# Kernel optimization log

Hardware: AMD Instinct MI355X
Metric: run time of the kernel (lower is better)

The kernel has to match this reference:

```python
import jax, jax.numpy as jnp
import numpy as np

N, E, H = 5000, 40000, 8
DIMS = [(258, 512), (516, 256), (262, 128), (136, 20)]  # (in_feature, out_feature) per GATDeformer


def setup_inputs() -> dict:
    key = jax.random.key(0)
    ks = jax.random.split(key, 10)
    s = 0.05
    data = jax.random.normal(ks[0], (N, 10), jnp.float32)
    src = jax.random.randint(ks[1], (E,), 0, N)
    off = jax.random.randint(ks[2], (E,), 1, N)
    edge_idx = jnp.stack([src, (src + off) % N]).astype(jnp.int32)  # no self loops by construction
    inp = {
        'data': data,
        'edge_idx': edge_idx,
        'W0': jax.random.normal(ks[3], (10, 256), jnp.float32) * s,
        'b0': jnp.zeros((256,), jnp.float32),
    }
    for i, (din, dout) in enumerate(DIMS, start=1):
        k = jax.random.split(ks[3 + i], 3)
        inp[f'W{i}'] = jax.random.normal(k[0], (din, H * dout), jnp.float32) * s
        inp[f'asrc{i}'] = jax.random.normal(k[1], (H, dout), jnp.float32) * s
        inp[f'adst{i}'] = jax.random.normal(k[2], (H, dout), jnp.float32) * s
        inp[f'bias{i}'] = jnp.zeros((dout,), jnp.float32)
    return inp


def _gat(x, src, dst, W, a_s, a_d, b):
    """PyG GATConv (concat=False): returns (mean-over-heads output + bias, alpha [E',H])."""
    Hh, C = a_s.shape
    h = (x @ W).reshape(N, Hh, C)                               # [N,H,C]
    e_s = jnp.einsum('nhc,hc->nh', h, a_s)                      # [N,H]
    e_d = jnp.einsum('nhc,hc->nh', h, a_d)
    logits = jax.nn.leaky_relu(e_s[src] + e_d[dst], 0.2)        # [E',H]
    m = jax.ops.segment_max(logits, dst, num_segments=N)        # segment softmax over incoming edges
    ex = jnp.exp(logits - m[dst])
    alpha = ex / jax.ops.segment_sum(ex, dst, num_segments=N)[dst]
    out = jax.ops.segment_sum(alpha[:, :, None] * h[src], dst, num_segments=N)  # [N,H,C]
    return out.mean(axis=1) + b, alpha


def _deformer(af, src, dst, W, a_s, a_d, b):
    # find_boundary on the layer input features
    up, down = af[:, 0] == 1.0, af[:, 0] == 0.0
    left, right = af[:, 1] == 0.0, af[:, 1] == 1.0
    feat, alpha = _gat(af, src, dst, W, a_s, a_d, b)
    coord = af[:, :2]
    # second propagate: alpha*0.2 reused to aggregate source coordinates, then mean over heads
    msg = (alpha * 0.2)[:, :, None] * coord[src][:, None, :]    # [E',H,2]
    oc = jax.ops.segment_sum(msg, dst, num_segments=N).mean(axis=1)
    # fix_boundary (sequential overwrite order: up then down, left then right)
    c0 = jnp.where(down, 0.0, jnp.where(up, 1.0, oc[:, 0]))
    c1 = jnp.where(right, 1.0, jnp.where(left, 0.0, oc[:, 1]))
    return jnp.stack([c0, c1], axis=1), jax.nn.selu(feat)


def reference(data, edge_idx, W0, b0, W1, asrc1, adst1, bias1, W2, asrc2, adst2, bias2, W3, asrc3, adst3, bias3, W4, asrc4, adst4, bias4):
    sl = jnp.arange(N, dtype=edge_idx.dtype)
    src = jnp.concatenate([edge_idx[0], sl])   # GATConv add_self_loops=True
    dst = jnp.concatenate([edge_idx[1], sl])
    coord = data[:, :2]
    feat = jax.nn.selu(data @ W0 + b0)
    c1_, f1 = _deformer(jnp.concatenate([coord, feat], 1), src, dst, W1, asrc1, adst1, bias1)
    c2_, f2 = _deformer(jnp.concatenate([c1_, coord, f1], 1), src, dst, W2, asrc2, adst2, bias2)
    c3_, f3 = _deformer(jnp.concatenate([c2_, c1_, coord, f2], 1), src, dst, W3, asrc3, adst3, bias3)
    c4_, _ = _deformer(jnp.concatenate([c3_, c2_, c1_, coord, f3], 1), src, dst, W4, asrc4, adst4, bias4)
    return c4_
```

## Files before the change

kernel.cpp:

```cpp
#include <hip/hip_runtime.h>

#define N_NODES 5000
#define NH 8

typedef unsigned short u16;
typedef short bf16x8 __attribute__((ext_vector_type(8)));
typedef float f32x4 __attribute__((ext_vector_type(4)));

static __device__ __forceinline__ float selu_f(float x) {
    const float sc = 1.0507009873554805f;
    const float al = 1.6732632423543772f;
    return x > 0.f ? sc * x : sc * al * (__expf(x) - 1.f);
}

static __device__ __forceinline__ u16 f2bf(float x) {
    union { float f; unsigned u; } v; v.f = x;
    unsigned r = v.u + 0x7fff + ((v.u >> 16) & 1);
    return (u16)(r >> 16);
}

static __device__ __forceinline__ float bf2f(unsigned hi16) {
    union { unsigned u; float f; } v; v.u = hi16 << 16;
    return v.f;
}

#define GL2LDS16(gp, lp)                                                        \
    __builtin_amdgcn_global_load_lds(                                           \
        (const __attribute__((address_space(1))) void*)(gp),                    \
        (__attribute__((address_space(3))) void*)(lp), 16, 0, 0)

__global__ void k_count(const int* __restrict__ ei, int* cnt, int E, int Esz) {
    int e = blockIdx.x * 256 + threadIdx.x;
    if (e >= Esz) return;
    int dst = (e < E) ? ei[E + e] : (e - E);
    atomicAdd(&cnt[dst], 1);
}

__global__ void k_scan(const int* __restrict__ cnt, int* __restrict__ rowp, int n) {
    __shared__ int ps[256];
    int t = threadIdx.x;
    int per = (n + 255) / 256;
    int b = t * per;
    int s = 0;
    for (int i = 0; i < per; ++i) { int idx = b + i; if (idx < n) s += cnt[idx]; }
    ps[t] = s;
    __syncthreads();
    for (int off = 1; off < 256; off <<= 1) {
        int v = (t >= off) ? ps[t - off] : 0;
        __syncthreads();
        ps[t] += v;
        __syncthreads();
    }
    int run = (t == 0) ? 0 : ps[t - 1];
    for (int i = 0; i < per; ++i) {
        int idx = b + i;
        if (idx < n) { rowp[idx] = run; run += cnt[idx]; }
    }
    if (t == 255) rowp[n] = run;
}

__global__ void k_fill(const int* __restrict__ ei, const int* __restrict__ rowp,
                       int* cur, int* ssrc, int E, int Esz) {
    int e = blockIdx.x * 256 + threadIdx.x;
    if (e >= Esz) return;
    int src, dst;
    if (e < E) { src = ei[e]; dst = ei[E + e]; }
    else       { src = e - E; dst = src; }
    int pos = rowp[dst] + atomicAdd(&cur[dst], 1);
    ssrc[pos] = src;
}

__global__ __launch_bounds__(256) void k_prep(
        const float* W1, const float* W2, const float* W3, const float* W4,
        const float* s1, const float* s2, const float* s3, const float* s4,
        const float* d1, const float* d2, const float* d3, const float* d4,
        float* __restrict__ fsAll, float* __restrict__ fdAll,
        u16* T1, u16* T2, u16* T3) {
    const int Ks[4] = {258, 516, 262, 136};
    const int Cs[4] = {512, 256, 128, 20};
    int bid = blockIdx.x;
    if (bid < 516) {
        int li = bid / 129;
        int k = (bid % 129) * 4 + (threadIdx.x >> 6);
        int lane = threadIdx.x & 63;
        if (k >= Ks[li]) return;
        const float* W  = (li == 0) ? W1 : (li == 1) ? W2 : (li == 2) ? W3 : W4;
        const float* as = (li == 0) ? s1 : (li == 1) ? s2 : (li == 2) ? s3 : s4;
        const float* ad = (li == 0) ? d1 : (li == 1) ? d2 : (li == 2) ? d3 : d4;
        int C = Cs[li];
        float s[8] = {0.f,0.f,0.f,0.f,0.f,0.f,0.f,0.f};
        float d[8] = {0.f,0.f,0.f,0.f,0.f,0.f,0.f,0.f};
        const float* wr = W + (size_t)k * 8 * C;
        for (int c = lane; c < C; c += 64) {
            #pragma unroll
            for (int h = 0; h < 8; ++h) {
                float w = wr[h * C + c];
                s[h] += w * as[h * C + c];
                d[h] += w * ad[h * C + c];
            }
        }
        #pragma unroll
        for (int off = 32; off >= 1; off >>= 1) {
            #pragma unroll
            for (int h = 0; h < 8; ++h) {
                s[h] += __shfl_xor(s[h], off);
                d[h] += __shfl_xor(d[h], off);
            }
        }
        if (lane == 0) {
            float* fo = fsAll + (size_t)li * 516 * 8 + k * 8;
            float* go = fdAll + (size_t)li * 516 * 8 + k * 8;
            #pragma unroll
            for (int h = 0; h < 8; ++h) { fo[h] = s[h]; go[h] = d[h]; }
        }
    } else {
        const int Kps[3] = {288, 544, 288};
        int w = bid - 516;
        int li = w / (16 * 136);
        int rem = w % (16 * 136);
        int c0 = (rem % 16) * 32;
        int j0 = (rem / 16) * 32;
        int C = Cs[li], K = Ks[li], Kp = Kps[li], KK = 8 * Kp;
        if (c0 >= C || j0 >= KK) return;
        const float* W = (li == 0) ? W1 : (li == 1) ? W2 : W3;
        u16* Wt2 = (li == 0) ? T1 : (li == 1) ? T2 : T3;
        __shared__ float tile[32][33];
        int h = j0 / Kp, k0 = j0 % Kp;
        int tid = threadIdx.x;
        for (int idx = tid; idx < 1024; idx += 256) {
            int kr = idx >> 5, cc = idx & 31;
            int gk = k0 + kr;
            tile[kr][cc] = (gk < K) ? W[(size_t)gk * (8 * C) + h * C + c0 + cc] : 0.f;
        }
        __syncthreads();
        for (int idx = tid; idx < 1024; idx += 256) {
            int cr = idx >> 5, kc = idx & 31;
            Wt2[(size_t)(c0 + cr) * KK + j0 + kc] = f2bf(tile[kc][cr]);
        }
    }
}

__global__ __launch_bounds__(256) void k_mf(const float* p0, const float* p1,
                                            const float* p2, const float* p3, int np,
                                            const float* __restrict__ data,
                                            const float* __restrict__ W0,
                                            const float* __restrict__ b0,
                                            const u16* __restrict__ facc,
                                            const float* __restrict__ biasp,
                                            int split, int MN, int FC, int K, int Kp,
                                            const float* __restrict__ fs,
                                            const float* __restrict__ fd,
                                            u16* __restrict__ afb,
                                            float* __restrict__ es, float* __restrict__ ed,
                                            float* __restrict__ c0out) {
    int n = blockIdx.x, t = threadIdx.x;
    __shared__ float drow[10];
    bool l1 = (biasp == nullptr);
    if (l1 && t < 10) drow[t] = data[n * 10 + t];
    __syncthreads();
    float pes[8] = {0.f,0.f,0.f,0.f,0.f,0.f,0.f,0.f};
    float ped[8] = {0.f,0.f,0.f,0.f,0.f,0.f,0.f,0.f};
    u16* rowb = afb + (size_t)n * Kp;
    for (int cf2 = t; 2 * cf2 < FC; cf2 += 256) {
        int cf = 2 * cf2;
        float v0, v1;
        if (l1) {
            float2 bb = *(const float2*)(b0 + cf);
            v0 = bb.x; v1 = bb.y;
            #pragma unroll
            for (int k = 0; k < 10; ++k) {
                float2 ww = *(const float2*)(W0 + k * 256 + cf);
                v0 += drow[k] * ww.x;
                v1 += drow[k] * ww.y;
            }
            v0 = selu_f(v0); v1 = selu_f(v1);
        } else {
            float s0 = 0.f, s1 = 0.f;
            for (int z = 0; z < split; ++z) {
                unsigned pr = *(const unsigned*)(facc + (size_t)z * MN + (size_t)n * FC + cf);
                s0 += bf2f(pr & 0xffff);
                s1 += bf2f(pr >> 16);
            }
            float2 bb = *(const float2*)(biasp + cf);
            v0 = selu_f(s0 * 0.125f + bb.x);
            v1 = selu_f(s1 * 0.125f + bb.y);
        }
        int c = 2 * np + cf;
        *(unsigned*)(rowb + c) = (unsigned)f2bf(v0) | ((unsigned)f2bf(v1) << 16);
        const float* fsr = fs + c * 8;
        const float* fdr = fd + c * 8;
        #pragma unroll
        for (int h = 0; h < 8; ++h) {
            pes[h] += v0 * fsr[h] + v1 * fsr[8 + h];
            ped[h] += v0 * fdr[h] + v1 * fdr[8 + h];
        }
    }
    if (t < 2 * np) {
        float v;
        if (l1) {
            v = drow[t];
            c0out[n * 2 + t] = v;
        } else {
            const float* p = (t < 2) ? p0 : (t < 4) ? p1 : (t < 6) ? p2 : p3;
            v = p[n * 2 + (t & 1)];
        }
        rowb[t] = f2bf(v);
        #pragma unroll
        for (int h = 0; h < 8; ++h) { pes[h] += v * fs[t * 8 + h]; ped[h] += v * fd[t * 8 + h]; }
    }
    for (int c = K + t; c < Kp; c += 256) rowb[c] = 0;
    #pragma unroll
    for (int off = 32; off >= 1; off >>= 1) {
        #pragma unroll
        for (int h = 0; h < 8; ++h) {
            pes[h] += __shfl_xor(pes[h], off);
            ped[h] += __shfl_xor(ped[h], off);
        }
    }
    __shared__ float red[4][16];
    int wv = t >> 6, ln = t & 63;
    if (ln == 0) {
        #pragma unroll
        for (int h = 0; h < 8; ++h) { red[wv][h] = pes[h]; red[wv][8 + h] = ped[h]; }
    }
    __syncthreads();
    if (t < 16) {
        float s = red[0][t] + red[1][t] + red[2][t] + red[3][t];
        if (t < 8) es[n * 8 + t] = s;
        else       ed[n * 8 + (t - 8)] = s;
    }
}

template <int S32>
__global__ __launch_bounds__(256) void k_gag(const float* __restrict__ es,
                            const float* __restrict__ ed,
                            const int* __restrict__ rowp, const int* __restrict__ ssrc,
                            const float* __restrict__ cprev, const u16* __restrict__ afb,
                            u16* __restrict__ g, float* __restrict__ cnext, int Kp) {
    __shared__ int   ls[128];
    __shared__ float la[128 * 8];
    __shared__ float lc0[128], lc1[128], lw[128];
    __shared__ float linv[8];
    int n = blockIdx.x, t = threadIdx.x;
    int s0 = rowp[n];
    int deg = rowp[n + 1] - s0;
    if (deg > 128) deg = 128;
    for (int i = t; i < deg; i += 256) {
        int src = ssrc[s0 + i];
        ls[i] = src;
        lc0[i] = cprev[src * 2];
        lc1[i] = cprev[src * 2 + 1];
    }
    __syncthreads();
    for (int i = t; i < deg * 8; i += 256) {
        int e = i >> 3, h = i & 7;
        float x = es[ls[e] * 8 + h] + ed[n * 8 + h];
        la[i] = x > 0.f ? x : 0.2f * x;
    }
    __syncthreads();
    if (t < 8) {
        float m = -1e30f;
        for (int e = 0; e < deg; ++e) m = fmaxf(m, la[e * 8 + t]);
        float s = 0.f;
        for (int e = 0; e < deg; ++e) {
            float v = __expf(la[e * 8 + t] - m);
            la[e * 8 + t] = v;
            s += v;
        }
        linv[t] = 1.f / s;
    }
    __syncthreads();
    for (int i = t; i < deg; i += 256) {
        float w = 0.f;
        #pragma unroll
        for (int h = 0; h < 8; ++h) w += la[i * 8 + h] * linv[h];
        lw[i] = w;
    }
    int nW = Kp >> 1;
    float acc[8][2 * S32];
    #pragma unroll
    for (int h = 0; h < 8; ++h)
        #pragma unroll
        for (int s = 0; s < 2 * S32; ++s) acc[h][s] = 0.f;
    int e = 0;
    for (; e + 3 < deg; e += 4) {
        const unsigned* r0 = (const unsigned*)(afb + (size_t)ls[e] * Kp);
        const unsigned* r1 = (const unsigned*)(afb + (size_t)ls[e + 1] * Kp);
        const unsigned* r2 = (const unsigned*)(afb + (size_t)ls[e + 2] * Kp);
        const unsigned* r3 = (const unsigned*)(afb + (size_t)ls[e + 3] * Kp);
        unsigned v0[S32], v1[S32], v2[S32], v3[S32];
        #pragma unroll
        for (int s = 0; s < S32; ++s) {
            int w = t + 256 * s;
            bool ok = (w < nW);
            v0[s] = ok ? r0[w] : 0u;
            v1[s] = ok ? r1[w] : 0u;
            v2[s] = ok ? r2[w] : 0u;
            v3[s] = ok ? r3[w] : 0u;
        }
        float a0[8], a1[8], a2[8], a3[8];
        #pragma unroll
        for (int h = 0; h < 8; ++h) {
            a0[h] = la[(e + 0) * 8 + h];
            a1[h] = la[(e + 1) * 8 + h];
            a2[h] = la[(e + 2) * 8 + h];
            a3[h] = la[(e + 3) * 8 + h];
        }
        #pragma unroll
        for (int s = 0; s < S32; ++s) {
            float x0 = bf2f(v0[s] & 0xffff), y0 = bf2f(v0[s] >> 16);
            float x1 = bf2f(v1[s] & 0xffff), y1 = bf2f(v1[s] >> 16);
            float x2 = bf2f(v2[s] & 0xffff), y2 = bf2f(v2[s] >> 16);
            float x3 = bf2f(v3[s] & 0xffff), y3 = bf2f(v3[s] >> 16);
            #pragma unroll
            for (int h = 0; h < 8; ++h) {
                acc[h][2 * s]     += a0[h] * x0 + a1[h] * x1 + a2[h] * x2 + a3[h] * x3;
                acc[h][2 * s + 1] += a0[h] * y0 + a1[h] * y1 + a2[h] * y2 + a3[h] * y3;
            }
        }
    }
    for (; e < deg; ++e) {
        const unsigned* r0 = (const unsigned*)(afb + (size_t)ls[e] * Kp);
        unsigned v0[S32];
        #pragma unroll
        for (int s = 0; s < S32; ++s) {
            int w = t + 256 * s;
            v0[s] = (w < nW) ? r0[w] : 0u;
        }
        float a0[8];
        #pragma unroll
        for (int h = 0; h < 8; ++h) a0[h] = la[e * 8 + h];
        #pragma unroll
        for (int s = 0; s < S32; ++s) {
            float x0 = bf2f(v0[s] & 0xffff), y0 = bf2f(v0[s] >> 16);
            #pragma unroll
            for (int h = 0; h < 8; ++h) {
                acc[h][2 * s]     += a0[h] * x0;
                acc[h][2 * s + 1] += a0[h] * y0;
            }
        }
    }
    unsigned* grw = (unsigned*)(g + (size_t)n * 8 * Kp);
    #pragma unroll
    for (int s = 0; s < S32; ++s) {
        int w = t + 256 * s;
        if (w < nW) {
            #pragma unroll
            for (int h = 0; h < 8; ++h) {
                float iv = linv[h];
                unsigned lo = f2bf(acc[h][2 * s] * iv);
                unsigned hi = f2bf(acc[h][2 * s + 1] * iv);
                grw[h * nW + w] = lo | (hi << 16);
            }
        }
    }
    __syncthreads();
    if (t == 0) {
        float oc0 = 0.f, oc1 = 0.f;
        for (int i = 0; i < deg; ++i) { oc0 += lw[i] * lc0[i]; oc1 += lw[i] * lc1[i]; }
        oc0 *= 0.025f; oc1 *= 0.025f;
        float a0 = cprev[n * 2], a1 = cprev[n * 2 + 1];
        cnext[n * 2]     = (a0 == 0.f) ? 0.f : ((a0 == 1.f) ? 1.f : oc0);
        cnext[n * 2 + 1] = (a1 == 1.f) ? 1.f : ((a1 == 0.f) ? 0.f : oc1);
    }
}

__global__ __launch_bounds__(256) void k_gemm_s(const u16* __restrict__ A,
                                                const u16* __restrict__ Bt,
                                                u16* __restrict__ facc16,
                                                int M, int KK, int NC, int kchunk, int MN) {
    __shared__ u16 As[3][128 * 32];
    __shared__ u16 Bs[3][128 * 32];
    int tid = threadIdx.x;
    int wave = tid >> 6, lane = tid & 63;
    int bm = blockIdx.y * 128, bn = blockIdx.x * 128, z = blockIdx.z;
    int kbeg = z * kchunk, kend = min(KK, kbeg + kchunk);
    int wm = (wave >> 1) * 64, wn = (wave & 1) * 64;
    int l16 = lane & 15, q = lane >> 4;
    f32x4 acc[4][4] = {};

    int seg0 = wave * 128 + lane;
    int seg1 = seg0 + 64;
    int row0 = seg0 >> 2, sq0 = (seg0 & 3) ^ (row0 & 3);
    int row1 = seg1 >> 2, sq1 = (seg1 & 3) ^ (row1 & 3);
    const u16* ga0 = A  + (size_t)(bm + row0) * KK + sq0 * 8;
    const u16* ga1 = A  + (size_t)(bm + row1) * KK + sq1 * 8;
    const u16* gb0 = Bt + (size_t)(bn + row0) * KK + sq0 * 8;
    const u16* gb1 = Bt + (size_t)(bn + row1) * KK + sq1 * 8;
    int lo0 = (wave * 2 + 0) * 512;
    int lo1 = (wave * 2 + 1) * 512;

#define STAGE_T(buf, kk)                          \
    do {                                          \
        GL2LDS16(ga0 + (kk), &As[buf][lo0]);      \
        GL2LDS16(ga1 + (kk), &As[buf][lo1]);      \
        GL2LDS16(gb0 + (kk), &Bs[buf][lo0]);      \
        GL2LDS16(gb1 + (kk), &Bs[buf][lo1]);      \
    } while (0)

    STAGE_T(0, kbeg);
    if (kbeg + 32 < kend) STAGE_T(1, kbeg + 32);
    int cur = 0;
    for (int k0 = kbeg; k0 < kend; k0 += 32) {
        if (k0 + 64 < kend) {
            int nb = cur + 2; if (nb >= 3) nb -= 3;
            STAGE_T(nb, k0 + 64);
            asm volatile("s_waitcnt vmcnt(8)" ::: "memory");
        } else if (k0 + 32 < kend) {
            asm volatile("s_waitcnt vmcnt(4)" ::: "memory");
        } else {
            asm volatile("s_waitcnt vmcnt(0)" ::: "memory");
        }
        __builtin_amdgcn_s_barrier();
        const u16* Asr = As[cur];
        const u16* Bsr = Bs[cur];
        bf16x8 fa[4], fb[4];
        #pragma unroll
        for (int mi = 0; mi < 4; ++mi) {
            int row = wm + mi * 16 + l16;
            fa[mi] = *(const bf16x8*)(Asr + row * 32 + ((q ^ (row & 3)) * 8));
            int col = wn + mi * 16 + l16;
            fb[mi] = *(const bf16x8*)(Bsr + col * 32 + ((q ^ (col & 3)) * 8));
        }
        #pragma unroll
        for (int mi = 0; mi < 4; ++mi)
            #pragma unroll
            for (int ni = 0; ni < 4; ++ni)
                acc[mi][ni] = __builtin_amdgcn_mfma_f32_16x16x32_bf16(fa[mi], fb[ni], acc[mi][ni], 0, 0, 0);
        __builtin_amdgcn_s_barrier();
        cur += 1; if (cur >= 3) cur -= 3;
    }
#undef STAGE_T
    u16* out = facc16 + (size_t)z * MN;
    #pragma unroll
    for (int mi = 0; mi < 4; ++mi) {
        int row0s = bm + wm + mi * 16 + q * 4;
        #pragma unroll
        for (int ni = 0; ni < 4; ++ni) {
            int col = bn + wn + ni * 16 + l16;
            #pragma unroll
            for (int r = 0; r < 4; ++r) {
                int row = row0s + r;
                if (row < M) out[(size_t)row * NC + col] = f2bf(acc[mi][ni][r]);
            }
        }
    }
}

__global__ void k_final(const float* __restrict__ es, const float* __restrict__ ed,
                        const int* __restrict__ rowp, const int* __restrict__ ssrc,
                        const float* __restrict__ cprev, float* __restrict__ outp) {
    int wid = (blockIdx.x * blockDim.x + threadIdx.x) >> 6;
    int lane = threadIdx.x & 63;
    if (wid >= N_NODES) return;
    int n = wid;
    int s0 = rowp[n], deg = rowp[n + 1] - s0;
    int h = lane & 7, ei = lane >> 3;
    float edh = ed[n * 8 + h];
    float m = -1e30f;
    for (int b = 0; b < deg; b += 8) {
        int e = b + ei;
        if (e < deg) {
            int src = ssrc[s0 + e];
            float x = es[src * 8 + h] + edh;
            x = x > 0.f ? x : 0.2f * x;
            m = fmaxf(m, x);
        }
    }
    m = fmaxf(m, __shfl_xor(m, 8));
    m = fmaxf(m, __shfl_xor(m, 16));
    m = fmaxf(m, __shfl_xor(m, 32));
    float ssum = 0.f;
    for (int b = 0; b < deg; b += 8) {
        int e = b + ei;
        if (e < deg) {
            int src = ssrc[s0 + e];
            float x = es[src * 8 + h] + edh;
            x = x > 0.f ? x : 0.2f * x;
            ssum += __expf(x - m);
        }
    }
    ssum += __shfl_xor(ssum, 8);
    ssum += __shfl_xor(ssum, 16);
    ssum += __shfl_xor(ssum, 32);
    float inv = 1.f / ssum;
    float oc0 = 0.f, oc1 = 0.f;
    for (int b = 0; b < deg; b += 8) {
        int e = b + ei;
        if (e < deg) {
            int src = ssrc[s0 + e];
            float x = es[src * 8 + h] + edh;
            x = x > 0.f ? x : 0.2f * x;
            float w = __expf(x - m) * inv;
            w += __shfl_xor(w, 1);
            w += __shfl_xor(w, 2);
            w += __shfl_xor(w, 4);
            if (h == 0) {
                oc0 += w * cprev[src * 2];
                oc1 += w * cprev[src * 2 + 1];
            }
        }
    }
    oc0 += __shfl_xor(oc0, 8);  oc1 += __shfl_xor(oc1, 8);
    oc0 += __shfl_xor(oc0, 16); oc1 += __shfl_xor(oc1, 16);
    oc0 += __shfl_xor(oc0, 32); oc1 += __shfl_xor(oc1, 32);
    if (lane == 0) {
        oc0 *= 0.025f; oc1 *= 0.025f;
        float a0 = cprev[n * 2], a1 = cprev[n * 2 + 1];
        outp[n * 2]     = (a0 == 0.f) ? 0.f : ((a0 == 1.f) ? 1.f : oc0);
        outp[n * 2 + 1] = (a1 == 1.f) ? 1.f : ((a1 == 0.f) ? 0.f : oc1);
    }
}

extern "C" void kernel_launch(void* const* d_in, const int* in_sizes, int n_in,
                              void* d_out, int out_size, void* d_ws, size_t ws_size,
                              hipStream_t stream) {
    const float* data = (const float*)d_in[0];
    const int* ei = (const int*)d_in[1];
    const float* W0 = (const float*)d_in[2];
    const float* b0 = (const float*)d_in[3];
    int E = in_sizes[1] / 2;
    int Esz = E + N_NODES;

    char* wp = (char*)d_ws;
    size_t off = 0;
    auto alloc = [&](size_t bytes) {
        void* p = wp + off;
        off += (bytes + 1023) & ~(size_t)1023;
        return p;
    };
    u16*   g     = (u16*)alloc((size_t)N_NODES * 8 * 576 * 2);
    u16*   T1    = (u16*)alloc((size_t)512 * 8 * 288 * 2);
    u16*   T2    = (u16*)alloc((size_t)256 * 8 * 544 * 2);
    u16*   T3    = (u16*)alloc((size_t)128 * 8 * 288 * 2);
    u16*   facc  = (u16*)alloc((size_t)8 * N_NODES * 512 * 2);
    u16*   afb   = (u16*)alloc((size_t)N_NODES * 576 * 2);
    float* es    = (float*)alloc((size_t)N_NODES * 8 * 4);
    float* ebd   = (float*)alloc((size_t)N_NODES * 8 * 4);
    float* fsAll = (float*)alloc((size_t)4 * 516 * 8 * 4);
    float* fdAll = (float*)alloc((size_t)4 * 516 * 8 * 4);
    float* c0    = (float*)alloc(N_NODES * 2 * 4);
    float* c1    = (float*)alloc(N_NODES * 2 * 4);
    float* c2    = (float*)alloc(N_NODES * 2 * 4);
    float* c3    = (float*)alloc(N_NODES * 2 * 4);
    int* cnt  = (int*)alloc(N_NODES * 2 * 4);
    int* cur  = cnt + N_NODES;
    int* rowp = (int*)alloc((N_NODES + 1) * 4);
    int* ssrc = (int*)alloc(Esz * 4);

    hipMemsetAsync(cnt, 0, N_NODES * 2 * 4, stream);
    int gE = (Esz + 255) / 256;
    k_count<<<gE, 256, 0, stream>>>(ei, cnt, E, Esz);
    k_scan<<<1, 256, 0, stream>>>(cnt, rowp, N_NODES);
    k_fill<<<gE, 256, 0, stream>>>(ei, rowp, cur, ssrc, E, Esz);

    struct LP { const float *W, *as, *ad, *bs; int K, C, split; };
    LP L[4] = {
        {(const float*)d_in[4],  (const float*)d_in[5],  (const float*)d_in[6],  (const float*)d_in[7],  258, 512, 4},
        {(const float*)d_in[8],  (const float*)d_in[9],  (const float*)d_in[10], (const float*)d_in[11], 516, 256, 8},
        {(const float*)d_in[12], (const float*)d_in[13], (const float*)d_in[14], (const float*)d_in[15], 262, 128, 8},
        {(const float*)d_in[16], (const float*)d_in[17], (const float*)d_in[18], (const float*)d_in[19], 136, 20, 1},
    };
    k_prep<<<516 + 16 * 136 * 3, 256, 0, stream>>>(
        L[0].W, L[1].W, L[2].W, L[3].W,
        L[0].as, L[1].as, L[2].as, L[3].as,
        L[0].ad, L[1].ad, L[2].ad, L[3].ad,
        fsAll, fdAll, T1, T2, T3);

    float* cbuf[4] = {c0, c1, c2, c3};
    u16* Tb[3] = {T1, T2, T3};
    int FC[4] = {256, 512, 256, 128};

    for (int li = 0; li < 4; ++li) {
        LP& lp = L[li];
        const float* p[4] = {nullptr, nullptr, nullptr, nullptr};
        for (int j = 0; j <= li; ++j) p[j] = cbuf[li - j];
        int Kp = ((lp.K + 31) / 32) * 32;
        int KK = 8 * Kp;
        const float* biasp = (li == 0) ? nullptr : L[li - 1].bs;
        int splitp = (li == 0) ? 1 : L[li - 1].split;
        int MNp = N_NODES * FC[li];
        const float* fs = fsAll + (size_t)li * 516 * 8;
        const float* fd = fdAll + (size_t)li * 516 * 8;

        k_mf<<<N_NODES, 256, 0, stream>>>(p[0], p[1], p[2], p[3], li + 1,
                                          data, W0, b0, facc, biasp, splitp, MNp, FC[li],
                                          lp.K, Kp, fs, fd, afb, es, ebd, c0);
        if (li < 3) {
            if ((Kp >> 1) <= 256)
                k_gag<1><<<N_NODES, 256, 0, stream>>>(es, ebd, rowp, ssrc, cbuf[li], afb,
                                                      g, cbuf[li + 1], Kp);
            else
                k_gag<2><<<N_NODES, 256, 0, stream>>>(es, ebd, rowp, ssrc, cbuf[li], afb,
                                                      g, cbuf[li + 1], Kp);
            int MN = N_NODES * lp.C;
            k_gemm_s<<<dim3(lp.C / 128, (N_NODES + 127) / 128, lp.split), 256, 0, stream>>>(
                g, Tb[li], facc, N_NODES, KK, lp.C, KK / lp.split, MN);
        } else {
            k_final<<<(N_NODES + 3) / 4, 256, 0, stream>>>(es, ebd, rowp, ssrc, cbuf[3],
                                                           (float*)d_out);
        }
    }
}
```

Measured before the change: 363.2 us.

## Process one destination node per wavefront in gather-aggregate kernel

Rewrites the attention-weighted gather kernel so each 64-lane wavefront handles one node instead of a 256-thread block per node. Four nodes share a block, block-wide barriers become wave-local LDS waits, and the softmax max/sum use wave shuffles across 8 lanes per head instead of 8 serial threads. The coordinate aggregation is also parallelised across lanes with a shuffle reduction instead of a single-thread loop. In exchange each lane now holds 3 or 5 packed words per edge, which raises register pressure, and the template is picked by a hardcoded Kp check.

```diff
diff --git a/kernel.cpp b/kernel.cpp
--- a/kernel.cpp
+++ b/kernel.cpp
@@ -28,6 +28,8 @@
     __builtin_amdgcn_global_load_lds(                                           \
         (const __attribute__((address_space(1))) void*)(gp),                    \
         (__attribute__((address_space(3))) void*)(lp), 16, 0, 0)
+
+#define WAVE_LDS_FENCE() asm volatile("s_waitcnt lgkmcnt(0)" ::: "memory")
 
 __global__ void k_count(const int* __restrict__ ei, int* cnt, int E, int Esz) {
     int e = blockIdx.x * 256 + threadIdx.x;
@@ -231,67 +233,79 @@
     }
 }
 
-template <int S32>
-__global__ __launch_bounds__(256) void k_gag(const float* __restrict__ es,
+template <int S>
+__global__ __launch_bounds__(256) void k_gag2(const float* __restrict__ es,
                             const float* __restrict__ ed,
                             const int* __restrict__ rowp, const int* __restrict__ ssrc,
                             const float* __restrict__ cprev, const u16* __restrict__ afb,
                             u16* __restrict__ g, float* __restrict__ cnext, int Kp) {
-    __shared__ int   ls[128];
-    __shared__ float la[128 * 8];
-    __shared__ float lc0[128], lc1[128], lw[128];
-    __shared__ float linv[8];
-    int n = blockIdx.x, t = threadIdx.x;
+    __shared__ float la_s[4][128 * 8];
+    __shared__ int   ls_s[4][128];
+    __shared__ float linv_s[4][8];
+    int w4 = threadIdx.x >> 6, lane = threadIdx.x & 63;
+    int n = blockIdx.x * 4 + w4;
+    if (n >= N_NODES) return;
+    float* la = la_s[w4];
+    int*   ls = ls_s[w4];
+    float* linv = linv_s[w4];
+
     int s0 = rowp[n];
     int deg = rowp[n + 1] - s0;
     if (deg > 128) deg = 128;
-    for (int i = t; i < deg; i += 256) {
-        int src = ssrc[s0 + i];
-        ls[i] = src;
-        lc0[i] = cprev[src * 2];
-        lc1[i] = cprev[src * 2 + 1];
-    }
-    __syncthreads();
-    for (int i = t; i < deg * 8; i += 256) {
-        int e = i >> 3, h = i & 7;
-        float x = es[ls[e] * 8 + h] + ed[n * 8 + h];
-        la[i] = x > 0.f ? x : 0.2f * x;
-    }
-    __syncthreads();
-    if (t < 8) {
-        float m = -1e30f;
-        for (int e = 0; e < deg; ++e) m = fmaxf(m, la[e * 8 + t]);
-        float s = 0.f;
-        for (int e = 0; e < deg; ++e) {
-            float v = __expf(la[e * 8 + t] - m);
-            la[e * 8 + t] = v;
-            s += v;
-        }
-        linv[t] = 1.f / s;
-    }
-    __syncthreads();
-    for (int i = t; i < deg; i += 256) {
-        float w = 0.f;
-        #pragma unroll
-        for (int h = 0; h < 8; ++h) w += la[i * 8 + h] * linv[h];
-        lw[i] = w;
-    }
+    for (int i = lane; i < deg; i += 64) ls[i] = ssrc[s0 + i];
+    WAVE_LDS_FENCE();
+
+    int h = lane & 7, ei = lane >> 3;
+    float edh = ed[n * 8 + h];
+    float m = -1e30f;
+    for (int b = 0; b < deg; b += 8) {
+        int e = b + ei;
+        if (e < deg) {
+            float x = es[ls[e] * 8 + h] + edh;
+            x = x > 0.f ? x : 0.2f * x;
+            la[e * 8 + h] = x;
+            m = fmaxf(m, x);
+        }
+    }
+    m = fmaxf(m, __shfl_xor(m, 8));
+    m = fmaxf(m, __shfl_xor(m, 16));
+    m = fmaxf(m, __shfl_xor(m, 32));
+    WAVE_LDS_FENCE();
+    float ssum = 0.f;
+    for (int b = 0; b < deg; b += 8) {
+        int e = b + ei;
+        if (e < deg) {
+            float v = __expf(la[e * 8 + h] - m);
+            la[e * 8 + h] = v;
+            ssum += v;
+        }
+    }
+    ssum += __shfl_xor(ssum, 8);
+    ssum += __shfl_xor(ssum, 16);
+    ssum += __shfl_xor(ssum, 32);
+    if (lane < 8) linv[lane] = 1.f / ssum;
+    WAVE_LDS_FENCE();
+
     int nW = Kp >> 1;
-    float acc[8][2 * S32];
+    float linv8[8];
     #pragma unroll
-    for (int h = 0; h < 8; ++h)
-        #pragma unroll
-        for (int s = 0; s < 2 * S32; ++s) acc[h][s] = 0.f;
+    for (int h2 = 0; h2 < 8; ++h2) linv8[h2] = linv[h2];
+
+    float acc[8][2 * S];
+    #pragma unroll
+    for (int h2 = 0; h2 < 8; ++h2)
+        #pragma unroll
+        for (int s = 0; s < 2 * S; ++s) acc[h2][s] = 0.f;
     int e = 0;
     for (; e + 3 < deg; e += 4) {
         const unsigned* r0 = (const unsigned*)(afb + (size_t)ls[e] * Kp);
         const unsigned* r1 = (const unsigned*)(afb + (size_t)ls[e + 1] * Kp);
         const unsigned* r2 = (const unsigned*)(afb + (size_t)ls[e + 2] * Kp);
         const unsigned* r3 = (const unsigned*)(afb + (size_t)ls[e + 3] * Kp);
-        unsigned v0[S32], v1[S32], v2[S32], v3[S32];
-        #pragma unroll
-        for (int s = 0; s < S32; ++s) {
-            int w = t + 256 * s;
+        unsigned v0[S], v1[S], v2[S], v3[S];
+        #pragma unroll
+        for (int s = 0; s < S; ++s) {
+            int w = lane + 64 * s;
             bool ok = (w < nW);
             v0[s] = ok ? r0[w] : 0u;
             v1[s] = ok ? r1[w] : 0u;
@@ -300,64 +314,75 @@
         }
         float a0[8], a1[8], a2[8], a3[8];
         #pragma unroll
-        for (int h = 0; h < 8; ++h) {
-            a0[h] = la[(e + 0) * 8 + h];
-            a1[h] = la[(e + 1) * 8 + h];
-            a2[h] = la[(e + 2) * 8 + h];
-            a3[h] = la[(e + 3) * 8 + h];
-        }
-        #pragma unroll
-        for (int s = 0; s < S32; ++s) {
+        for (int h2 = 0; h2 < 8; ++h2) {
+            a0[h2] = la[(e + 0) * 8 + h2];
+            a1[h2] = la[(e + 1) * 8 + h2];
+            a2[h2] = la[(e + 2) * 8 + h2];
+            a3[h2] = la[(e + 3) * 8 + h2];
+        }
+        #pragma unroll
+        for (int s = 0; s < S; ++s) {
             float x0 = bf2f(v0[s] & 0xffff), y0 = bf2f(v0[s] >> 16);
             float x1 = bf2f(v1[s] & 0xffff), y1 = bf2f(v1[s] >> 16);
             float x2 = bf2f(v2[s] & 0xffff), y2 = bf2f(v2[s] >> 16);
             float x3 = bf2f(v3[s] & 0xffff), y3 = bf2f(v3[s] >> 16);
             #pragma unroll
-            for (int h = 0; h < 8; ++h) {
-                acc[h][2 * s]     += a0[h] * x0 + a1[h] * x1 + a2[h] * x2 + a3[h] * x3;
-                acc[h][2 * s + 1] += a0[h] * y0 + a1[h] * y1 + a2[h] * y2 + a3[h] * y3;
+            for (int h2 = 0; h2 < 8; ++h2) {
+                acc[h2][2 * s]     += a0[h2] * x0 + a1[h2] * x1 + a2[h2] * x2 + a3[h2] * x3;
+                acc[h2][2 * s + 1] += a0[h2] * y0 + a1[h2] * y1 + a2[h2] * y2 + a3[h2] * y3;
             }
         }
     }
     for (; e < deg; ++e) {
         const unsigned* r0 = (const unsigned*)(afb + (size_t)ls[e] * Kp);
-        unsigned v0[S32];
-        #pragma unroll
-        for (int s = 0; s < S32; ++s) {
-            int w = t + 256 * s;
+        unsigned v0[S];
+        #pragma unroll
+        for (int s = 0; s < S; ++s) {
+            int w = lane + 64 * s;
             v0[s] = (w < nW) ? r0[w] : 0u;
         }
         float a0[8];
         #pragma unroll
-        for (int h = 0; h < 8; ++h) a0[h] = la[e * 8 + h];
-        #pragma unroll
-        for (int s = 0; s < S32; ++s) {
+        for (int h2 = 0; h2 < 8; ++h2) a0[h2] = la[e * 8 + h2];
+        #pragma unroll
+        for (int s = 0; s < S; ++s) {
             float x0 = bf2f(v0[s] & 0xffff), y0 = bf2f(v0[s] >> 16);
             #pragma unroll
-            for (int h = 0; h < 8; ++h) {
-                acc[h][2 * s]     += a0[h] * x0;
-                acc[h][2 * s + 1] += a0[h] * y0;
+            for (int h2 = 0; h2 < 8; ++h2) {
+                acc[h2][2 * s]     += a0[h2] * x0;
+                acc[h2][2 * s + 1] += a0[h2] * y0;
             }
         }
     }
     unsigned* grw = (unsigned*)(g + (size_t)n * 8 * Kp);
     #pragma unroll
-    for (int s = 0; s < S32; ++s) {
-        int w = t + 256 * s;
+    for (int s = 0; s < S; ++s) {
+        int w = lane + 64 * s;
         if (w < nW) {
             #pragma unroll
-            for (int h = 0; h < 8; ++h) {
-                float iv = linv[h];
-                unsigned lo = f2bf(acc[h][2 * s] * iv);
-                unsigned hi = f2bf(acc[h][2 * s + 1] * iv);
-                grw[h * nW + w] = lo | (hi << 16);
-            }
-        }
-    }
-    __syncthreads();
-    if (t == 0) {
-        float oc0 = 0.f, oc1 = 0.f;
-        for (int i = 0; i < deg; ++i) { oc0 += lw[i] * lc0[i]; oc1 += lw[i] * lc1[i]; }
+            for (int h2 = 0; h2 < 8; ++h2) {
+                float iv = linv8[h2];
+                unsigned lo = f2bf(acc[h2][2 * s] * iv);
+                unsigned hi = f2bf(acc[h2][2 * s + 1] * iv);
+                grw[h2 * nW + w] = lo | (hi << 16);
+            }
+        }
+    }
+    float oc0 = 0.f, oc1 = 0.f;
+    for (int i = lane; i < deg; i += 64) {
+        float wsum = 0.f;
+        #pragma unroll
+        for (int h2 = 0; h2 < 8; ++h2) wsum += la[i * 8 + h2] * linv8[h2];
+        int src = ls[i];
+        oc0 += wsum * cprev[src * 2];
+        oc1 += wsum * cprev[src * 2 + 1];
+    }
+    #pragma unroll
+    for (int off = 1; off <= 32; off <<= 1) {
+        oc0 += __shfl_xor(oc0, off);
+        oc1 += __shfl_xor(oc1, off);
+    }
+    if (lane == 0) {
         oc0 *= 0.025f; oc1 *= 0.025f;
         float a0 = cprev[n * 2], a1 = cprev[n * 2 + 1];
         cnext[n * 2]     = (a0 == 0.f) ? 0.f : ((a0 == 1.f) ? 1.f : oc0);
@@ -587,12 +612,13 @@
                                           data, W0, b0, facc, biasp, splitp, MNp, FC[li],
                                           lp.K, Kp, fs, fd, afb, es, ebd, c0);
         if (li < 3) {
-            if ((Kp >> 1) <= 256)
-                k_gag<1><<<N_NODES, 256, 0, stream>>>(es, ebd, rowp, ssrc, cbuf[li], afb,
-                                                      g, cbuf[li + 1], Kp);
+            int gG = (N_NODES + 3) / 4;
+            if (Kp == 544)
+                k_gag2<5><<<gG, 256, 0, stream>>>(es, ebd, rowp, ssrc, cbuf[li], afb,
+                                                  g, cbuf[li + 1], Kp);
             else
-                k_gag<2><<<N_NODES, 256, 0, stream>>>(es, ebd, rowp, ssrc, cbuf[li], afb,
-                                                      g, cbuf[li + 1], Kp);
+                k_gag2<3><<<gG, 256, 0, stream>>>(es, ebd, rowp, ssrc, cbuf[li], afb,
+                                                  g, cbuf[li + 1], Kp);
             int MN = N_NODES * lp.C;
             k_gemm_s<<<dim3(lp.C / 128, (N_NODES + 127) / 128, lp.split), 256, 0, stream>>>(
                 g, Tb[li], facc, N_NODES, KK, lp.C, KK / lp.split, MN);
```

After: 359.3 us. About the same (-1.1%).
